# Kernel optimization log

Measured on AMD Instinct MI355X. Metric: run time of the kernel, lower is better.

The kernel has to match this reference:

```python
import jax, jax.numpy as jnp
import numpy as np

N, E, G, H, D = 50000, 800000, 64, 2, 128  # nodes, edges, graphs, heads, out_channels
NEG_SLOPE_ATT = 0.2   # GATv2 default negative_slope
NEG_SLOPE_OUT = 0.01  # torch.nn.LeakyReLU default
BN_EPS = 1e-5


def setup_inputs() -> dict:
    key = jax.random.key(0)
    ks = jax.random.split(key, 12)
    x = jax.random.normal(ks[0], (N, 1), jnp.float32)
    edge_index = jax.random.randint(ks[1], (2, E), 0, N, dtype=jnp.int64)
    edge_attr = jax.random.normal(ks[2], (E,), jnp.float32)
    batch = jnp.sort(jax.random.randint(ks[3], (N,), 0, G, dtype=jnp.int64))
    # GATv2Conv params: lin_l/lin_r: Linear(1, H*D) with bias; lin_edge: Linear(1, H*D) no bias
    Wl = jax.random.normal(ks[4], (1, H * D), jnp.float32) * 0.5
    bl = jax.random.normal(ks[5], (H * D,), jnp.float32) * 0.1
    Wr = jax.random.normal(ks[6], (1, H * D), jnp.float32) * 0.5
    br = jax.random.normal(ks[7], (H * D,), jnp.float32) * 0.1
    We = jax.random.normal(ks[8], (1, H * D), jnp.float32) * 0.5
    att = jax.random.normal(ks[9], (H, D), jnp.float32) * 0.5
    bias = jax.random.normal(ks[10], (D,), jnp.float32) * 0.1
    gamma = jnp.ones((D,), jnp.float32)
    beta = jnp.zeros((D,), jnp.float32)
    return {"x": x, "edge_index": edge_index, "edge_attr": edge_attr, "batch": batch,
            "Wl": Wl, "bl": bl, "Wr": Wr, "br": br, "We": We, "att": att,
            "bias": bias, "gamma": gamma, "beta": beta}


def reference(x, edge_index, edge_attr, batch, Wl, bl, Wr, br, We, att, bias, gamma, beta):
    n = x.shape[0]
    src, dst = edge_index[0], edge_index[1]  # message flows src -> dst
    # node transforms: [N, H, D]
    xl = (x @ Wl + bl).reshape(n, H, D)  # lin_l (source side, also the message value)
    xr = (x @ Wr + br).reshape(n, H, D)  # lin_r (destination side)
    # edge feature embedding: [E, H, D]
    ee = (edge_attr[:, None] @ We).reshape(-1, H, D)
    # GATv2 scoring: leaky_relu(x_j + x_i + e), then dot with attention vector
    m = jax.nn.leaky_relu(xl[src] + xr[dst] + ee, NEG_SLOPE_ATT)  # [E, H, D]
    alpha = jnp.einsum('ehd,hd->eh', m, att)  # [E, H]
    # scatter-softmax over incoming edges per destination node
    amax = jax.ops.segment_max(alpha, dst, num_segments=n)  # [N, H]
    ea = jnp.exp(alpha - amax[dst])
    denom = jax.ops.segment_sum(ea, dst, num_segments=n)
    alpha = ea / (denom[dst] + 1e-16)
    # weighted scatter-add aggregation of x_j
    out = jax.ops.segment_sum(xl[src] * alpha[..., None], dst, num_segments=n)  # [N, H, D]
    out = out.mean(axis=1) + bias  # concat=False -> head average, then conv bias
    # BatchNorm1d in training mode (biased variance over nodes)
    mean = out.mean(axis=0)
    var = ((out - mean) ** 2).mean(axis=0)
    out = (out - mean) * jax.lax.rsqrt(var + BN_EPS) * gamma + beta
    out = jax.nn.leaky_relu(out, NEG_SLOPE_OUT)
    # graph-level scatter_add pooling
    return jax.ops.segment_sum(out, batch, num_segments=G)  # [G, D]
```

## Files before the change

### kernel.cpp

```cpp
#include <hip/hip_runtime.h>
#include <math.h>

#define NN 50000
#define NE 800000
#define NG 64

#define CB    1024
#define NBLK  782
#define NBUCK 196

static_assert(NBLK * CB >= NE, "chunk cover");
static_assert((NBUCK - 1) == (NN - 1) / 256, "bucket count");
static_assert(NE % 4 == 0, "edge unroll");

#define WS_C     0
#define WS_ACC   16
#define WS_BNSUM (WS_ACC + 4*NN)
#define WS_BNSQ  (WS_BNSUM + 128)
#define WS_MOM   WS_BNSUM
#define WS_EX    (WS_BNSQ + 128)
#define WS_TOT   (WS_EX + 272)
#define WS_BSUM  (WS_TOT + 256)
#define WS_CNT   (WS_BSUM + 256)
#define WS_SORT  (WS_CNT + 256*NBLK)
#define WS_END   (WS_SORT + 4*NE)
#define WS_NEED_BYTES ((size_t)WS_END * 4 + 256)

static_assert(((WS_SORT * 4) % 16) == 0, "sort 16B alignment");

#define STEP(wl_, wr_, we_, bb_, at_, xs_, xd_, ae_, acc_)                 \
  { float tt = fmaf(we_, ae_, bb_); tt = fmaf(wr_, xd_, tt);               \
    tt = fmaf(wl_, xs_, tt); acc_ = fmaf(fabsf(tt), at_, acc_); }

#define SMEM_WEIGHTS_DECL                                                  \
  __shared__ __align__(16) float sWl[256], sWr[256], sWe[256], sB[256], sAt[256];

#define SMEM_WEIGHTS_LOAD                                                  \
  { int t_ = threadIdx.x;                                                  \
    sWl[t_] = Wl[t_]; sWr[t_] = Wr[t_]; sWe[t_] = We[t_];                  \
    sB[t_] = bl[t_] + br[t_]; sAt[t_] = att[t_]; }                         \
  __syncthreads();

#define SCORES(xs_, xd_, ae_, accA, accB, out0, out1)                      \
  { float lin0 = fmaf(c0.x, xs_, fmaf(c0.y, xd_, fmaf(c0.z, ae_, c0.w))); \
    out0 = fmaf(0.4f, accA, 0.6f * lin0);                                  \
    float lin1 = fmaf(c1.x, xs_, fmaf(c1.y, xd_, fmaf(c1.z, ae_, c1.w))); \
    out1 = fmaf(0.4f, accB, 0.6f * lin1); }

#define STEP4(c, q0, q1, q2, q3)                                           \
  STEP(wl.c, wr.c, we.c, bb.c, at.c, xs0, xd0, ae0, q0)                    \
  STEP(wl.c, wr.c, we.c, bb.c, at.c, xs1, xd1, ae1, q1)                    \
  STEP(wl.c, wr.c, we.c, bb.c, at.c, xs2, xd2, ae2, q2)                    \
  STEP(wl.c, wr.c, we.c, bb.c, at.c, xs3, xd3, ae3, q3)

#define SCORE_CORE                                                         \
  int4 s4 = *(const int4*)&ei[base];                                       \
  int4 dd4 = *(const int4*)&ei[NE + base];                                 \
  float4 ae4 = *(const float4*)&eattr[base];                               \
  float xs0 = x[s4.x], xs1 = x[s4.y], xs2 = x[s4.z], xs3 = x[s4.w];        \
  float xd0 = x[dd4.x], xd1 = x[dd4.y], xd2 = x[dd4.z], xd3 = x[dd4.w];    \
  float ae0 = ae4.x, ae1 = ae4.y, ae2 = ae4.z, ae3 = ae4.w;

#define SCORE_LOOPS                                                        \
  float a00 = 0.f, a01 = 0.f, a02 = 0.f, a03 = 0.f;                        \
  float a10 = 0.f, a11 = 0.f, a12 = 0.f, a13 = 0.f;                        \
  _Pragma("unroll 2")                                                      \
  for (int j = 0; j < 128; j += 4) {                                       \
    float4 wl = *(const float4*)&sWl[j];                                   \
    float4 wr = *(const float4*)&sWr[j];                                   \
    float4 we = *(const float4*)&sWe[j];                                   \
    float4 bb = *(const float4*)&sB[j];                                    \
    float4 at = *(const float4*)&sAt[j];                                   \
    STEP4(x, a00, a01, a02, a03)                                           \
    STEP4(y, a00, a01, a02, a03)                                           \
    STEP4(z, a00, a01, a02, a03)                                           \
    STEP4(w, a00, a01, a02, a03)                                           \
  }                                                                        \
  _Pragma("unroll 2")                                                      \
  for (int j = 128; j < 256; j += 4) {                                     \
    float4 wl = *(const float4*)&sWl[j];                                   \
    float4 wr = *(const float4*)&sWr[j];                                   \
    float4 we = *(const float4*)&sWe[j];                                   \
    float4 bb = *(const float4*)&sB[j];                                    \
    float4 at = *(const float4*)&sAt[j];                                   \
    STEP4(x, a10, a11, a12, a13)                                           \
    STEP4(y, a10, a11, a12, a13)                                           \
    STEP4(z, a10, a11, a12, a13)                                           \
    STEP4(w, a10, a11, a12, a13)                                           \
  }                                                                        \
  float4 c0 = *(const float4*)&ws[WS_C];                                   \
  float4 c1 = *(const float4*)&ws[WS_C + 4];

extern "C" __global__ __launch_bounds__(256)
void k_hist(const int* __restrict__ ei,
            const float* __restrict__ att, const float* __restrict__ Wl,
            const float* __restrict__ Wr, const float* __restrict__ We,
            const float* __restrict__ bl, const float* __restrict__ br,
            float* __restrict__ ws, float* __restrict__ out)
{
  __shared__ unsigned cnt[256];
  cnt[threadIdx.x] = 0u;
  __syncthreads();
  int base = blockIdx.x * CB + (int)threadIdx.x * 4;
  if (base < NE) {
    int4 a = *(const int4*)&ei[NE + base];
    atomicAdd(&cnt[((unsigned)a.x) >> 8], 1u);
    atomicAdd(&cnt[((unsigned)a.y) >> 8], 1u);
    atomicAdd(&cnt[((unsigned)a.z) >> 8], 1u);
    atomicAdd(&cnt[((unsigned)a.w) >> 8], 1u);
  }
  __syncthreads();
  unsigned* counts = (unsigned*)(ws + WS_CNT);
  counts[(size_t)threadIdx.x * NBLK + blockIdx.x] = cnt[threadIdx.x];
  int gid = blockIdx.x * 256 + (int)threadIdx.x;
  if (gid < NG * 128) out[gid] = 0.f;
  if (gid < 14) ws[WS_MOM + gid] = 0.f;
  if (blockIdx.x == 0) {
    int t = threadIdx.x;
    ws[WS_BSUM + t] = bl[t] + br[t];
    __shared__ float red[4][256];
    float a = att[t];
    red[0][t] = a * Wl[t];
    red[1][t] = a * Wr[t];
    red[2][t] = a * We[t];
    red[3][t] = a * (bl[t] + br[t]);
    __syncthreads();
    if (t < 8) {
      int k = t >> 1, h = t & 1;
      float s = 0.f;
      for (int d = 0; d < 128; ++d) s += red[k][h * 128 + d];
      ws[WS_C + h * 4 + k] = s;
    }
  }
}

extern "C" __global__ __launch_bounds__(256)
void k_scan1(float* __restrict__ ws)
{
  int b = blockIdx.x;
  int t = threadIdx.x;
  unsigned* row = (unsigned*)(ws + WS_CNT) + (size_t)b * NBLK;
  __shared__ unsigned sc[256];
  unsigned carry = 0;
  for (int c = 0; c < NBLK; c += 256) {
    int k = c + t;
    unsigned v = (k < NBLK) ? row[k] : 0u;
    sc[t] = v;
    __syncthreads();
    for (int o = 1; o < 256; o <<= 1) {
      unsigned u = (t >= o) ? sc[t - o] : 0u;
      __syncthreads();
      sc[t] += u;
      __syncthreads();
    }
    unsigned incl = sc[t];
    if (k < NBLK) row[k] = carry + incl - v;
    unsigned total = sc[255];
    __syncthreads();
    carry += total;
  }
  if (t == 0) ((unsigned*)(ws + WS_TOT))[b] = carry;
}

extern "C" __global__ __launch_bounds__(256)
void k_scan2(float* __restrict__ ws)
{
  int b = threadIdx.x;
  unsigned v = ((const unsigned*)(ws + WS_TOT))[b];
  __shared__ unsigned sc[256];
  sc[b] = v;
  __syncthreads();
  for (int o = 1; o < 256; o <<= 1) {
    unsigned u = (b >= o) ? sc[b - o] : 0u;
    __syncthreads();
    sc[b] += u;
    __syncthreads();
  }
  unsigned* ex = (unsigned*)(ws + WS_EX);
  ex[b] = sc[b] - v;
  if (b == 255) ex[256] = sc[b];
}

extern "C" __global__ __launch_bounds__(256, 2)
void k_score(const int* __restrict__ ei, const float* __restrict__ x,
             const float* __restrict__ eattr,
             const float* __restrict__ Wl, const float* __restrict__ Wr,
             const float* __restrict__ We, const float* __restrict__ att,
             const float* __restrict__ bsum,
             float* __restrict__ ws)
{
  __shared__ unsigned soff[256];
  { int t_ = threadIdx.x;
    const unsigned* counts = (const unsigned*)(ws + WS_CNT);
    const unsigned* ex = (const unsigned*)(ws + WS_EX);
    soff[t_] = ex[t_] + counts[(size_t)t_ * NBLK + blockIdx.x];
  }
  __syncthreads();
  int base = blockIdx.x * CB + (int)threadIdx.x * 4;
  if (base >= NE) return;
  SCORE_CORE
  float a00 = 0.f, a01 = 0.f, a02 = 0.f, a03 = 0.f;
  float a10 = 0.f, a11 = 0.f, a12 = 0.f, a13 = 0.f;
#pragma unroll 2
  for (int j = 0; j < 128; j += 4) {
    float4 wl = *(const float4*)&Wl[j];
    float4 wr = *(const float4*)&Wr[j];
    float4 we = *(const float4*)&We[j];
    float4 bb = *(const float4*)&bsum[j];
    float4 at = *(const float4*)&att[j];
    STEP4(x, a00, a01, a02, a03)
    STEP4(y, a00, a01, a02, a03)
    STEP4(z, a00, a01, a02, a03)
    STEP4(w, a00, a01, a02, a03)
  }
#pragma unroll 2
  for (int j = 128; j < 256; j += 4) {
    float4 wl = *(const float4*)&Wl[j];
    float4 wr = *(const float4*)&Wr[j];
    float4 we = *(const float4*)&We[j];
    float4 bb = *(const float4*)&bsum[j];
    float4 at = *(const float4*)&att[j];
    STEP4(x, a10, a11, a12, a13)
    STEP4(y, a10, a11, a12, a13)
    STEP4(z, a10, a11, a12, a13)
    STEP4(w, a10, a11, a12, a13)
  }
  float4 c0 = *(const float4*)&ws[WS_C];
  float4 c1 = *(const float4*)&ws[WS_C + 4];
  float4* srt = (float4*)(ws + WS_SORT);
  float s0, s1;
#define EPI(i, dv, qa, qb)                                                 \
  { SCORES(xs##i, xd##i, ae##i, qa, qb, s0, s1)                            \
    unsigned d_ = (unsigned)(dv);                                          \
    unsigned p_ = atomicAdd(&soff[d_ >> 8], 1u);                           \
    srt[p_] = make_float4(__expf(s0), __expf(s1), xs##i, __uint_as_float(d_)); }
  EPI(0, dd4.x, a00, a10) EPI(1, dd4.y, a01, a11)
  EPI(2, dd4.z, a02, a12) EPI(3, dd4.w, a03, a13)
#undef EPI
}

extern "C" __global__ __launch_bounds__(256)
void k_gather(float* __restrict__ ws)
{
  int b = blockIdx.x;
  const int t = threadIdx.x;
  __shared__ float acc[1024];
  acc[t] = 0.f; acc[256 + t] = 0.f; acc[512 + t] = 0.f; acc[768 + t] = 0.f;
  __syncthreads();
  const unsigned* ex = (const unsigned*)(ws + WS_EX);
  int lo = (int)ex[b], hi = (int)ex[b + 1];
  const float4* srt = (const float4*)(ws + WS_SORT);
  for (int i = lo + t; i < hi; i += 256) {
    float4 r = srt[i];
    int l4 = (int)(__float_as_uint(r.w) & 255u) * 4;
    atomicAdd(&acc[l4 + 0], r.x);
    atomicAdd(&acc[l4 + 1], r.y);
    atomicAdd(&acc[l4 + 2], r.x * r.z);
    atomicAdd(&acc[l4 + 3], r.y * r.z);
  }
  __syncthreads();
  int n = (b << 8) + t;
  float f1 = 0.f, f2 = 0.f, f3 = 0.f, f4 = 0.f;
  if (n < NN) {
    float4 A = make_float4(acc[t * 4], acc[t * 4 + 1], acc[t * 4 + 2], acc[t * 4 + 3]);
    *(float4*)&ws[WS_ACC + 4 * n] = A;
    float r0 = 1.f / (A.x + 1e-16f);
    float r1 = 1.f / (A.y + 1e-16f);
    f1 = A.x * r0; f2 = A.z * r0; f3 = A.y * r1; f4 = A.w * r1;
  }
  float pm[14] = { f1, f2, f3, f4,
                   f1*f1, f1*f2, f1*f3, f1*f4,
                   f2*f2, f2*f3, f2*f4,
                   f3*f3, f3*f4, f4*f4 };
#pragma unroll
  for (int k = 0; k < 14; ++k) {
    float v = pm[k];
#pragma unroll
    for (int m = 32; m >= 1; m >>= 1) v += __shfl_xor(v, m);
    pm[k] = v;
  }
  __shared__ float smom[56];
  int wid = t >> 6, lane = t & 63;
  if (lane == 0) {
#pragma unroll
    for (int k = 0; k < 14; ++k) smom[wid * 14 + k] = pm[k];
  }
  __syncthreads();
  if (t < 14) {
    float s = smom[t] + smom[14 + t] + smom[28 + t] + smom[42 + t];
    atomicAdd(&ws[WS_MOM + t], s);
  }
}

extern "C" __global__ __launch_bounds__(256)
void k4m_pool(const int* __restrict__ batch,
              const float* __restrict__ Wl, const float* __restrict__ bl,
              const float* __restrict__ bias, const float* __restrict__ gamma,
              const float* __restrict__ beta,
              float* __restrict__ ws, float* __restrict__ out)
{
  const int CHUNK = (NN + (int)gridDim.x - 1) / (int)gridDim.x;
  int n0 = blockIdx.x * CHUNK;
  if (n0 >= NN) return;
  int n1 = n0 + CHUNK; if (n1 > NN) n1 = NN;
  int t = threadIdx.x;
  int d = t & 127;
  int row = t >> 7;
  float S1 = ws[WS_MOM + 0], S2 = ws[WS_MOM + 1];
  float S3 = ws[WS_MOM + 2], S4 = ws[WS_MOM + 3];
  float M11 = ws[WS_MOM + 4], M12 = ws[WS_MOM + 5], M13 = ws[WS_MOM + 6];
  float M14 = ws[WS_MOM + 7], M22 = ws[WS_MOM + 8], M23 = ws[WS_MOM + 9];
  float M24 = ws[WS_MOM + 10], M33 = ws[WS_MOM + 11], M34 = ws[WS_MOM + 12];
  float M44 = ws[WS_MOM + 13];
  float g1 = 0.5f * bl[d], g2 = 0.5f * Wl[d];
  float g3 = 0.5f * bl[128 + d], g4 = 0.5f * Wl[128 + d];
  float g5 = bias[d];
  const float invN = 1.f / (float)NN;
  float dotS = g1 * S1 + g2 * S2 + g3 * S3 + g4 * S4;
  float mean = (dotS + (float)NN * g5) * invN;
  float sumsq = g1*g1*M11 + g2*g2*M22 + g3*g3*M33 + g4*g4*M44
              + 2.f*(g1*g2*M12 + g1*g3*M13 + g1*g4*M14
                   + g2*g3*M23 + g2*g4*M24 + g3*g4*M34)
              + 2.f*g5*dotS + (float)NN*g5*g5;
  float var = fmaf(sumsq, invN, -mean * mean);
  float scale = gamma[d] * rsqrtf(var + 1e-5f);
  float shift = fmaf(-mean, scale, beta[d]);
  __shared__ float pool[4][128];
  for (int i = t; i < 512; i += 256) ((float*)pool)[i] = 0.f;
  __syncthreads();
  int g0 = batch[n0];
  for (int n = n0 + row; n < n1; n += 2) {
    float4 a = *(const float4*)&ws[WS_ACC + 4 * n];
    float r0 = 1.f / (a.x + 1e-16f);
    float r1 = 1.f / (a.y + 1e-16f);
    float o = g1 * (a.x * r0) + g2 * (a.z * r0)
            + g3 * (a.y * r1) + g4 * (a.w * r1) + g5;
    float v = fmaf(o, scale, shift);
    v = v > 0.f ? v : 0.01f * v;
    int g = batch[n];
    int slot = g - g0;
    if (slot < 4) atomicAdd(&pool[slot][d], v);
    else atomicAdd(&out[g * 128 + d], v);
  }
  __syncthreads();
  for (int i = t; i < 512; i += 256) {
    int slot = i >> 7, dd = i & 127;
    int g = g0 + slot;
    float v = pool[slot][dd];
    if (g < NG && v != 0.f) atomicAdd(&out[g * 128 + dd], v);
  }
}

extern "C" __global__ __launch_bounds__(256)
void k0_init(float* __restrict__ ws,
             const float* __restrict__ att, const float* __restrict__ Wl,
             const float* __restrict__ Wr, const float* __restrict__ We,
             const float* __restrict__ bl, const float* __restrict__ br,
             float* __restrict__ out)
{
  int tid = blockIdx.x * 256 + threadIdx.x;
  int nt = gridDim.x * 256;
  for (int i = tid; i < 4 * NN; i += nt) ws[WS_ACC + i] = 0.f;
  for (int i = tid; i < 256; i += nt) ws[WS_BNSUM + i] = 0.f;
  for (int i = tid; i < NG * 128; i += nt) out[i] = 0.f;
  if (blockIdx.x == 0) {
    __shared__ float red[4][256];
    int t = threadIdx.x;
    float a = att[t];
    red[0][t] = a * Wl[t];
    red[1][t] = a * Wr[t];
    red[2][t] = a * We[t];
    red[3][t] = a * (bl[t] + br[t]);
    __syncthreads();
    if (t < 8) {
      int k = t >> 1, h = t & 1;
      float s = 0.f;
      for (int d = 0; d < 128; ++d) s += red[k][h * 128 + d];
      ws[WS_C + h * 4 + k] = s;
    }
  }
}

extern "C" __global__ __launch_bounds__(256)
void k12f(const int* __restrict__ ei, const float* __restrict__ x,
          const float* __restrict__ eattr,
          const float* __restrict__ Wl, const float* __restrict__ Wr,
          const float* __restrict__ We, const float* __restrict__ bl,
          const float* __restrict__ br, const float* __restrict__ att,
          float* __restrict__ ws)
{
  SMEM_WEIGHTS_DECL
  SMEM_WEIGHTS_LOAD
  int base = (blockIdx.x * 256 + threadIdx.x) * 4;
  if (base >= NE) return;
  SCORE_CORE
  SCORE_LOOPS
  float* acc = ws + WS_ACC;
  float s0, s1;
#define EPI2(xs_, xd_, ae_, accA, accB, dsti)                              \
  { SCORES(xs_, xd_, ae_, accA, accB, s0, s1)                              \
    float e0 = __expf(s0), e1 = __expf(s1);                                \
    float* a = &acc[4 * dsti];                                             \
    atomicAdd(a + 0, e0); atomicAdd(a + 1, e1);                            \
    atomicAdd(a + 2, e0 * xs_); atomicAdd(a + 3, e1 * xs_); }
  EPI2(xs0, xd0, ae0, a00, a10, dd4.x)
  EPI2(xs1, xd1, ae1, a01, a11, dd4.y)
  EPI2(xs2, xd2, ae2, a02, a12, dd4.z)
  EPI2(xs3, xd3, ae3, a03, a13, dd4.w)
#undef EPI2
}

__device__ __forceinline__ float node_out4(float4 a, float wl0, float wl1,
                                           float b0, float b1, float bs)
{
  float r0 = 1.f / (a.x + 1e-16f);
  float r1 = 1.f / (a.y + 1e-16f);
  return 0.5f * (fmaf(wl0, a.z * r0, b0 * (a.x * r0)) +
                 fmaf(wl1, a.w * r1, b1 * (a.y * r1))) + bs;
}

extern "C" __global__ __launch_bounds__(256)
void k3_stats(const float* __restrict__ Wl, const float* __restrict__ bl,
              const float* __restrict__ bias, float* __restrict__ ws)
{
  int d = threadIdx.x & 127;
  int row = threadIdx.x >> 7;
  float wl0 = Wl[d], wl1 = Wl[128 + d];
  float b0 = bl[d], b1 = bl[128 + d];
  float bs = bias[d];
  float sum = 0.f, sq = 0.f;
  for (int n = blockIdx.x * 2 + row; n < NN; n += gridDim.x * 2) {
    float4 a = *(const float4*)&ws[WS_ACC + 4 * n];
    float o = node_out4(a, wl0, wl1, b0, b1, bs);
    sum += o;
    sq = fmaf(o, o, sq);
  }
  __shared__ float l1[256], l2[256];
  l1[threadIdx.x] = sum; l2[threadIdx.x] = sq;
  __syncthreads();
  if (row == 0) {
    atomicAdd(&ws[WS_BNSUM + d], l1[d] + l1[128 + d]);
    atomicAdd(&ws[WS_BNSQ + d], l2[d] + l2[128 + d]);
  }
}

extern "C" __global__ __launch_bounds__(256)
void k4_pool(const int* __restrict__ batch,
             const float* __restrict__ Wl, const float* __restrict__ bl,
             const float* __restrict__ bias, const float* __restrict__ gamma,
             const float* __restrict__ beta,
             float* __restrict__ ws, float* __restrict__ out)
{
  const int CHUNK = (NN + (int)gridDim.x - 1) / (int)gridDim.x;
  int n0 = blockIdx.x * CHUNK;
  if (n0 >= NN) return;
  int n1 = n0 + CHUNK; if (n1 > NN) n1 = NN;
  int d = threadIdx.x & 127;
  int row = threadIdx.x >> 7;
  const float invN = 1.f / (float)NN;
  float mean = ws[WS_BNSUM + d] * invN;
  float var = fmaf(ws[WS_BNSQ + d], invN, -mean * mean);
  float scale = gamma[d] * rsqrtf(var + 1e-5f);
  float shift = fmaf(-mean, scale, beta[d]);
  float wl0 = Wl[d], wl1 = Wl[128 + d];
  float b0 = bl[d], b1 = bl[128 + d];
  float bs = bias[d];
  __shared__ float pool[4][128];
  for (int i = threadIdx.x; i < 512; i += 256) ((float*)pool)[i] = 0.f;
  __syncthreads();
  int g0 = batch[n0];
  for (int n = n0 + row; n < n1; n += 2) {
    float4 a = *(const float4*)&ws[WS_ACC + 4 * n];
    float o = node_out4(a, wl0, wl1, b0, b1, bs);
    float v = fmaf(o, scale, shift);
    v = v > 0.f ? v : 0.01f * v;
    int g = batch[n];
    int slot = g - g0;
    if (slot < 4) atomicAdd(&pool[slot][d], v);
    else atomicAdd(&out[g * 128 + d], v);
  }
  __syncthreads();
  for (int i = threadIdx.x; i < 512; i += 256) {
    int slot = i >> 7, dd = i & 127;
    int g = g0 + slot;
    float v = pool[slot][dd];
    if (g < NG && v != 0.f) atomicAdd(&out[g * 128 + dd], v);
  }
}

extern "C" void kernel_launch(void* const* d_in, const int* in_sizes, int n_in,
                              void* d_out, int out_size, void* d_ws, size_t ws_size,
                              hipStream_t stream) {
  const float* x     = (const float*)d_in[0];
  const int*   ei    = (const int*)d_in[1];
  const float* eattr = (const float*)d_in[2];
  const int*   batch = (const int*)d_in[3];
  const float* Wl    = (const float*)d_in[4];
  const float* bl    = (const float*)d_in[5];
  const float* Wr    = (const float*)d_in[6];
  const float* br    = (const float*)d_in[7];
  const float* We    = (const float*)d_in[8];
  const float* att   = (const float*)d_in[9];
  const float* bias  = (const float*)d_in[10];
  const float* gam   = (const float*)d_in[11];
  const float* bet   = (const float*)d_in[12];
  float* ws  = (float*)d_ws;
  float* out = (float*)d_out;

  const bool dense = (ws_size >= WS_NEED_BYTES);

  if (dense) {
    hipLaunchKernelGGL(k_hist, dim3(NBLK), dim3(256), 0, stream,
                       ei, att, Wl, Wr, We, bl, br, ws, out);
    hipLaunchKernelGGL(k_scan1, dim3(256), dim3(256), 0, stream, ws);
    hipLaunchKernelGGL(k_scan2, dim3(1), dim3(256), 0, stream, ws);
    hipLaunchKernelGGL(k_score, dim3(NBLK), dim3(256), 0, stream,
                       ei, x, eattr, Wl, Wr, We, att,
                       (const float*)(ws + WS_BSUM), ws);
    hipLaunchKernelGGL(k_gather, dim3(NBUCK), dim3(256), 0, stream, ws);
    hipLaunchKernelGGL(k4m_pool, dim3(256), dim3(256), 0, stream,
                       batch, Wl, bl, bias, gam, bet, ws, out);
  } else {
    hipLaunchKernelGGL(k0_init, dim3(128), dim3(256), 0, stream,
                       ws, att, Wl, Wr, We, bl, br, out);
    hipLaunchKernelGGL(k12f, dim3((NE / 4 + 255) / 256), dim3(256), 0, stream,
                       ei, x, eattr, Wl, Wr, We, bl, br, att, ws);
    hipLaunchKernelGGL(k3_stats, dim3(256), dim3(256), 0, stream,
                       Wl, bl, bias, ws);
    hipLaunchKernelGGL(k4_pool, dim3(256), dim3(256), 0, stream,
                       batch, Wl, bl, bias, gam, bet, ws, out);
  }
}
```

Before: 189.6 us.

## Use packed 2-wide FMA for head scores and widen gather blocks to 1024

```diff
diff --git a/kernel.cpp b/kernel.cpp
--- a/kernel.cpp
+++ b/kernel.cpp
@@ -20,13 +20,26 @@
 #define WS_MOM   WS_BNSUM
 #define WS_EX    (WS_BNSQ + 128)
 #define WS_TOT   (WS_EX + 272)
-#define WS_BSUM  (WS_TOT + 256)
-#define WS_CNT   (WS_BSUM + 256)
+#define WS_PK    (WS_TOT + 256)
+#define WS_CNT   (WS_PK + 1280)
 #define WS_SORT  (WS_CNT + 256*NBLK)
 #define WS_END   (WS_SORT + 4*NE)
 #define WS_NEED_BYTES ((size_t)WS_END * 4 + 256)
 
 static_assert(((WS_SORT * 4) % 16) == 0, "sort 16B alignment");
+
+typedef float v2f __attribute__((ext_vector_type(2)));
+
+__device__ __forceinline__ v2f pkfma(v2f a, v2f b, v2f c) {
+#if __has_builtin(__builtin_elementwise_fma)
+  return __builtin_elementwise_fma(a, b, c);
+#else
+  v2f r; r.x = fmaf(a.x, b.x, c.x); r.y = fmaf(a.y, b.y, c.y); return r;
+#endif
+}
+__device__ __forceinline__ v2f pkabs(v2f a) {
+  v2f r; r.x = fabsf(a.x); r.y = fabsf(a.y); return r;
+}
 
 #define STEP(wl_, wr_, we_, bb_, at_, xs_, xd_, ae_, acc_)                 \
   { float tt = fmaf(we_, ae_, bb_); tt = fmaf(wr_, xd_, tt);               \
@@ -117,7 +130,12 @@
   if (gid < 14) ws[WS_MOM + gid] = 0.f;
   if (blockIdx.x == 0) {
     int t = threadIdx.x;
-    ws[WS_BSUM + t] = bl[t] + br[t];
+    int jj = (t >> 1) + ((t & 1) << 7);
+    ws[WS_PK +        t] = Wl[jj];
+    ws[WS_PK +  256 + t] = Wr[jj];
+    ws[WS_PK +  512 + t] = We[jj];
+    ws[WS_PK +  768 + t] = bl[jj] + br[jj];
+    ws[WS_PK + 1024 + t] = att[jj];
     __shared__ float red[4][256];
     float a = att[t];
     red[0][t] = a * Wl[t];
@@ -184,9 +202,7 @@
 extern "C" __global__ __launch_bounds__(256, 2)
 void k_score(const int* __restrict__ ei, const float* __restrict__ x,
              const float* __restrict__ eattr,
-             const float* __restrict__ Wl, const float* __restrict__ Wr,
-             const float* __restrict__ We, const float* __restrict__ att,
-             const float* __restrict__ bsum,
+             const float* __restrict__ pk,
              float* __restrict__ ws)
 {
   __shared__ unsigned soff[256];
@@ -199,58 +215,59 @@
   int base = blockIdx.x * CB + (int)threadIdx.x * 4;
   if (base >= NE) return;
   SCORE_CORE
-  float a00 = 0.f, a01 = 0.f, a02 = 0.f, a03 = 0.f;
-  float a10 = 0.f, a11 = 0.f, a12 = 0.f, a13 = 0.f;
+  v2f A0 = {0.f, 0.f}, A1 = A0, A2 = A0, A3 = A0;
+#define PKSTEP(wlp, wrp, wep, bbp, atp, xs_, xd_, ae_, acc_)               \
+  { v2f tt = pkfma(wep, (v2f){ae_, ae_}, bbp);                             \
+    tt = pkfma(wrp, (v2f){xd_, xd_}, tt);                                  \
+    tt = pkfma(wlp, (v2f){xs_, xs_}, tt);                                  \
+    acc_ = pkfma(pkabs(tt), atp, acc_); }
+#define PKSTEP4(wlp, wrp, wep, bbp, atp)                                   \
+  PKSTEP(wlp, wrp, wep, bbp, atp, xs0, xd0, ae0, A0)                       \
+  PKSTEP(wlp, wrp, wep, bbp, atp, xs1, xd1, ae1, A1)                       \
+  PKSTEP(wlp, wrp, wep, bbp, atp, xs2, xd2, ae2, A2)                       \
+  PKSTEP(wlp, wrp, wep, bbp, atp, xs3, xd3, ae3, A3)
 #pragma unroll 2
-  for (int j = 0; j < 128; j += 4) {
-    float4 wl = *(const float4*)&Wl[j];
-    float4 wr = *(const float4*)&Wr[j];
-    float4 we = *(const float4*)&We[j];
-    float4 bb = *(const float4*)&bsum[j];
-    float4 at = *(const float4*)&att[j];
-    STEP4(x, a00, a01, a02, a03)
-    STEP4(y, a00, a01, a02, a03)
-    STEP4(z, a00, a01, a02, a03)
-    STEP4(w, a00, a01, a02, a03)
-  }
-#pragma unroll 2
-  for (int j = 128; j < 256; j += 4) {
-    float4 wl = *(const float4*)&Wl[j];
-    float4 wr = *(const float4*)&Wr[j];
-    float4 we = *(const float4*)&We[j];
-    float4 bb = *(const float4*)&bsum[j];
-    float4 at = *(const float4*)&att[j];
-    STEP4(x, a10, a11, a12, a13)
-    STEP4(y, a10, a11, a12, a13)
-    STEP4(z, a10, a11, a12, a13)
-    STEP4(w, a10, a11, a12, a13)
-  }
+  for (int g = 0; g < 64; ++g) {
+    float4 wl = *(const float4*)&pk[       4 * g];
+    float4 wr = *(const float4*)&pk[ 256 + 4 * g];
+    float4 we = *(const float4*)&pk[ 512 + 4 * g];
+    float4 bb = *(const float4*)&pk[ 768 + 4 * g];
+    float4 at = *(const float4*)&pk[1024 + 4 * g];
+    v2f wlA = {wl.x, wl.y}, wrA = {wr.x, wr.y}, weA = {we.x, we.y};
+    v2f bbA = {bb.x, bb.y}, atA = {at.x, at.y};
+    v2f wlB = {wl.z, wl.w}, wrB = {wr.z, wr.w}, weB = {we.z, we.w};
+    v2f bbB = {bb.z, bb.w}, atB = {at.z, at.w};
+    PKSTEP4(wlA, wrA, weA, bbA, atA)
+    PKSTEP4(wlB, wrB, weB, bbB, atB)
+  }
+#undef PKSTEP4
+#undef PKSTEP
   float4 c0 = *(const float4*)&ws[WS_C];
   float4 c1 = *(const float4*)&ws[WS_C + 4];
   float4* srt = (float4*)(ws + WS_SORT);
   float s0, s1;
-#define EPI(i, dv, qa, qb)                                                 \
-  { SCORES(xs##i, xd##i, ae##i, qa, qb, s0, s1)                            \
+#define EPI(i, dv, Acc)                                                    \
+  { SCORES(xs##i, xd##i, ae##i, Acc.x, Acc.y, s0, s1)                      \
     unsigned d_ = (unsigned)(dv);                                          \
     unsigned p_ = atomicAdd(&soff[d_ >> 8], 1u);                           \
     srt[p_] = make_float4(__expf(s0), __expf(s1), xs##i, __uint_as_float(d_)); }
-  EPI(0, dd4.x, a00, a10) EPI(1, dd4.y, a01, a11)
-  EPI(2, dd4.z, a02, a12) EPI(3, dd4.w, a03, a13)
+  EPI(0, dd4.x, A0) EPI(1, dd4.y, A1)
+  EPI(2, dd4.z, A2) EPI(3, dd4.w, A3)
 #undef EPI
 }
 
-extern "C" __global__ __launch_bounds__(256)
+extern "C" __global__ __launch_bounds__(1024)
 void k_gather(float* __restrict__ ws)
 {
   int b = blockIdx.x;
   const int t = threadIdx.x;
   __shared__ float acc[1024];
-  acc[t] = 0.f; acc[256 + t] = 0.f; acc[512 + t] = 0.f; acc[768 + t] = 0.f;
+  acc[t] = 0.f;
   __syncthreads();
   const unsigned* ex = (const unsigned*)(ws + WS_EX);
   int lo = (int)ex[b], hi = (int)ex[b + 1];
   const float4* srt = (const float4*)(ws + WS_SORT);
-  for (int i = lo + t; i < hi; i += 256) {
+  for (int i = lo + t; i < hi; i += 1024) {
     float4 r = srt[i];
     int l4 = (int)(__float_as_uint(r.w) & 255u) * 4;
     atomicAdd(&acc[l4 + 0], r.x);
@@ -259,14 +276,16 @@
     atomicAdd(&acc[l4 + 3], r.y * r.z);
   }
   __syncthreads();
-  int n = (b << 8) + t;
   float f1 = 0.f, f2 = 0.f, f3 = 0.f, f4 = 0.f;
-  if (n < NN) {
-    float4 A = make_float4(acc[t * 4], acc[t * 4 + 1], acc[t * 4 + 2], acc[t * 4 + 3]);
-    *(float4*)&ws[WS_ACC + 4 * n] = A;
-    float r0 = 1.f / (A.x + 1e-16f);
-    float r1 = 1.f / (A.y + 1e-16f);
-    f1 = A.x * r0; f2 = A.z * r0; f3 = A.y * r1; f4 = A.w * r1;
+  if (t < 256) {
+    int n = (b << 8) + t;
+    if (n < NN) {
+      float4 A = make_float4(acc[t * 4], acc[t * 4 + 1], acc[t * 4 + 2], acc[t * 4 + 3]);
+      *(float4*)&ws[WS_ACC + 4 * n] = A;
+      float r0 = 1.f / (A.x + 1e-16f);
+      float r1 = 1.f / (A.y + 1e-16f);
+      f1 = A.x * r0; f2 = A.z * r0; f3 = A.y * r1; f4 = A.w * r1;
+    }
   }
   float pm[14] = { f1, f2, f3, f4,
                    f1*f1, f1*f2, f1*f3, f1*f4,
@@ -279,7 +298,7 @@
     for (int m = 32; m >= 1; m >>= 1) v += __shfl_xor(v, m);
     pm[k] = v;
   }
-  __shared__ float smom[56];
+  __shared__ float smom[224];
   int wid = t >> 6, lane = t & 63;
   if (lane == 0) {
 #pragma unroll
@@ -287,7 +306,9 @@
   }
   __syncthreads();
   if (t < 14) {
-    float s = smom[t] + smom[14 + t] + smom[28 + t] + smom[42 + t];
+    float s = 0.f;
+#pragma unroll
+    for (int w = 0; w < 16; ++w) s += smom[w * 14 + t];
     atomicAdd(&ws[WS_MOM + t], s);
   }
 }
@@ -515,9 +536,8 @@
     hipLaunchKernelGGL(k_scan1, dim3(256), dim3(256), 0, stream, ws);
     hipLaunchKernelGGL(k_scan2, dim3(1), dim3(256), 0, stream, ws);
     hipLaunchKernelGGL(k_score, dim3(NBLK), dim3(256), 0, stream,
-                       ei, x, eattr, Wl, Wr, We, att,
-                       (const float*)(ws + WS_BSUM), ws);
-    hipLaunchKernelGGL(k_gather, dim3(NBUCK), dim3(256), 0, stream, ws);
+                       ei, x, eattr, (const float*)(ws + WS_PK), ws);
+    hipLaunchKernelGGL(k_gather, dim3(NBUCK), dim3(1024), 0, stream, ws);
     hipLaunchKernelGGL(k4m_pool, dim3(256), dim3(256), 0, stream,
                        batch, Wl, bl, bias, gam, bet, ws, out);
   } else {
```

New measurement: 190.8 us. About the same (+0.6%).
